# Performance work log

Measured on AMD Instinct MI355X. Metric: run time of the kernel, lower is better.

The kernel has to match this reference:

```python
import jax, jax.numpy as jnp
import numpy as np


def setup_inputs() -> dict:
    key = jax.random.key(0)
    k1, k2, k3, k4, k5 = jax.random.split(key, 5)
    B, S, H, F, E = 2, 512, 1024, 3584, 8
    scale_in = 1.0 / np.sqrt(H)
    scale_ff = 1.0 / np.sqrt(F)
    return {
        "hidden_states": jax.random.normal(k1, (B, S, H), dtype=jnp.float32),
        "gate_w": jax.random.normal(k2, (E, H), dtype=jnp.float32) * scale_in,
        "w1": jax.random.normal(k3, (E, F, H), dtype=jnp.float32) * scale_in,
        "w2": jax.random.normal(k4, (E, H, F), dtype=jnp.float32) * scale_ff,
        "w3": jax.random.normal(k5, (E, F, H), dtype=jnp.float32) * scale_in,
    }


TOP_K = 2


def reference(hidden_states, gate_w, w1, w2, w3):
    B, S, H = hidden_states.shape
    E = gate_w.shape[0]
    x = hidden_states.reshape(B * S, H)  # [T, H]
    T = x.shape[0]

    # Router: softmax in fp32, top-2 selection, renormalize selected weights.
    router_logits = x @ gate_w.T  # [T, E]
    probs = jax.nn.softmax(router_logits.astype(jnp.float32), axis=-1)
    top_vals, top_idx = jax.lax.top_k(probs, TOP_K)  # [T, K]
    top_vals = top_vals / jnp.sum(top_vals, axis=-1, keepdims=True)
    top_vals = top_vals.astype(x.dtype)

    # Dense routing-weight matrix [T, E]: weight if selected else 0
    # (equivalent to the one-hot expert_mask + index_add combine).
    dense_w = jnp.zeros((T, E), dtype=x.dtype).at[
        jnp.arange(T)[:, None], top_idx
    ].add(top_vals)

    # Expert SwiGLU MLPs, batched over the expert axis.
    h1 = jnp.einsum("th,efh->etf", x, w1)  # [E, T, F]
    h3 = jnp.einsum("th,efh->etf", x, w3)  # [E, T, F]
    y = jnp.einsum("etf,ehf->eth", jax.nn.silu(h1) * h3, w2)  # [E, T, H]

    # Weighted combine across experts.
    out = jnp.einsum("eth,te->th", y, dense_w)  # [T, H]
    return out.reshape(B, S, H), router_logits
```

## Files before the change

### kernel.cpp

```cpp
#include <hip/hip_runtime.h>
#include <hip/hip_bf16.h>

typedef __bf16 v8bf __attribute__((ext_vector_type(8)));
typedef __bf16 v4bf __attribute__((ext_vector_type(4)));
typedef float  f32x4 __attribute__((ext_vector_type(4)));
typedef unsigned int u32;

#define NTOK 1024
#define HDIM 1024
#define FDIM 3584
#define NEXP 8
#define NPAIR 2048
#define MAXT 16
#define KSPLIT2 4
#define KPER2 (FDIM / KSPLIT2)

#define OFF_COUNTS   0
#define OFF_OFFSETS  64
#define OFF_NT1      128
#define OFF_T1E      192
#define OFF_T1M      320
#define OFF_TOKIDX   2048
#define OFF_TOKWT    (2048 + 4*NPAIR)
#define OFF_PAIRTOK  (OFF_TOKWT + 4*NPAIR)
#define OFF_PAIRWT   (OFF_PAIRTOK + 4*NPAIR)
#define OFF_SLOTOF   (OFF_PAIRWT + 4*NPAIR)
#define OFF_XB       65536
#define OFF_ACT      (OFF_XB + 2ull*NTOK*HDIM)
#define OFF_Y        (OFF_ACT + 2ull*NPAIR*FDIM)
#define YSTRIDE      ((size_t)NPAIR * HDIM)

static __device__ inline v4bf cvt4(float4 f) {
    v4bf r;
    r[0] = (__bf16)f.x; r[1] = (__bf16)f.y; r[2] = (__bf16)f.z; r[3] = (__bf16)f.w;
    return r;
}

static __device__ inline v8bf pack8(f32x4 lo, f32x4 hi) {
    v8bf r;
    r[0] = (__bf16)lo[0]; r[1] = (__bf16)lo[1]; r[2] = (__bf16)lo[2]; r[3] = (__bf16)lo[3];
    r[4] = (__bf16)hi[0]; r[5] = (__bf16)hi[1]; r[6] = (__bf16)hi[2]; r[7] = (__bf16)hi[3];
    return r;
}

#define FENCE() asm volatile("" ::: "memory")
#define BARRIER() do { FENCE(); __builtin_amdgcn_s_barrier(); FENCE(); } while (0)
#define WAITVM0() asm volatile("s_waitcnt vmcnt(0)" ::: "memory")
#define WAITLGKM0() asm volatile("s_waitcnt lgkmcnt(0)" ::: "memory")

#define DMA16(SRC, DST) \
    __builtin_amdgcn_global_load_lds((const __attribute__((address_space(1))) u32*)(SRC), \
                                     (__attribute__((address_space(3))) u32*)(DST), 16, 0, 0)

__global__ __launch_bounds__(256) void moe_cvtx(const float* __restrict__ x,
                                                __bf16* __restrict__ xb)
{
    const size_t i = ((size_t)blockIdx.x * 256 + threadIdx.x) * 4;
    float4 v = *(const float4*)(x + i);
    *(v4bf*)(xb + i) = cvt4(v);
}

__global__ __launch_bounds__(256) void moe_router(
    const float* __restrict__ x, const float* __restrict__ gw,
    float* __restrict__ logits, int* __restrict__ counts,
    int* __restrict__ tok_idx, float* __restrict__ tok_wt)
{
    const int lane = threadIdx.x & 63;
    const int wv = threadIdx.x >> 6;
    const int t = blockIdx.x * 4 + wv;
    const float* xr = x + (size_t)t * HDIM;

    float acc[NEXP];
#pragma unroll
    for (int e = 0; e < NEXP; ++e) acc[e] = 0.f;
#pragma unroll
    for (int j = 0; j < 4; ++j) {
        int h = lane * 4 + j * 256;
        float4 xv = *(const float4*)(xr + h);
#pragma unroll
        for (int e = 0; e < NEXP; ++e) {
            float4 g = *(const float4*)(gw + e * HDIM + h);
            acc[e] += xv.x * g.x + xv.y * g.y + xv.z * g.z + xv.w * g.w;
        }
    }
#pragma unroll
    for (int e = 0; e < NEXP; ++e) {
#pragma unroll
        for (int s = 32; s > 0; s >>= 1) acc[e] += __shfl_xor(acc[e], s);
    }
    if (lane == 0) {
#pragma unroll
        for (int e = 0; e < NEXP; ++e) logits[t * NEXP + e] = acc[e];
        int i0 = 0;
#pragma unroll
        for (int e = 1; e < NEXP; ++e) if (acc[e] > acc[i0]) i0 = e;
        int i1 = (i0 == 0) ? 1 : 0;
#pragma unroll
        for (int e = 0; e < NEXP; ++e) if (e != i0 && acc[e] > acc[i1]) i1 = e;
        float w0 = 1.f / (1.f + expf(acc[i1] - acc[i0]));
        float w1 = 1.f - w0;
        tok_idx[2 * t] = i0; tok_idx[2 * t + 1] = i1;
        tok_wt[2 * t] = w0;  tok_wt[2 * t + 1] = w1;
        atomicAdd(&counts[i0], 1);
        atomicAdd(&counts[i1], 1);
    }
}

__global__ void moe_scatter(const int* __restrict__ counts, const int* __restrict__ tok_idx,
                            const float* __restrict__ tok_wt, int* __restrict__ offsets,
                            int* __restrict__ pair_token, float* __restrict__ pair_wt,
                            int* __restrict__ slot_of,
                            int* __restrict__ t1e, int* __restrict__ t1m, int* __restrict__ nt1)
{
    __shared__ int cur[NEXP];
    const int tid = threadIdx.x;
    if (tid == 0) {
        int run = 0, n1 = 0;
        for (int e = 0; e < NEXP; ++e) {
            offsets[e] = run; cur[e] = run;
            for (int m0 = 0; m0 < counts[e]; m0 += 256) { t1e[n1] = e; t1m[n1] = m0; ++n1; }
            run += counts[e];
        }
        *nt1 = n1;
    }
    __syncthreads();
    for (int p = tid; p < 2 * NTOK; p += blockDim.x) {
        int e = tok_idx[p];
        int s = atomicAdd(&cur[e], 1);
        pair_token[s] = p >> 1;
        pair_wt[s] = tok_wt[p];
        slot_of[p] = s;
    }
}

__global__ __launch_bounds__(256, 2) void moe_gemm1(
    const __bf16* __restrict__ xb, const float* __restrict__ w1g,
    const float* __restrict__ w3g, const int* __restrict__ counts,
    const int* __restrict__ offsets, const int* __restrict__ pair_token,
    const int* __restrict__ t1e, const int* __restrict__ t1m,
    const int* __restrict__ nt1,
    __bf16* __restrict__ act)
{
    const int ty = blockIdx.y;
    if (ty >= *nt1) return;
    const int e = t1e[ty];
    const int m0 = t1m[ty];
    const int Me = counts[e];
    const int rows = min(256, Me - m0);
    const int slot0 = offsets[e] + m0;
    const int n0 = blockIdx.x * 64;

    __shared__ __align__(16) __bf16 As[256 * 32];
    __shared__ __align__(16) float  B1s[64 * 32];
    __shared__ __align__(16) float  B3s[64 * 32];

    const int tid = threadIdx.x;
    const int lane = tid & 63;
    const int wv = tid >> 6;
    const int ln4 = lane >> 4;
    const int lr = lane & 15;
    const int wm = (wv >> 1) * 128;
    const int wn = (wv & 1) * 32;

    f32x4 acc1[8][2], acc3[8][2];
#pragma unroll
    for (int i = 0; i < 8; ++i)
#pragma unroll
        for (int j = 0; j < 2; ++j) {
            acc1[i][j] = (f32x4){0.f, 0.f, 0.f, 0.f};
            acc3[i][j] = (f32x4){0.f, 0.f, 0.f, 0.f};
        }

    const char* asrc[4];
#pragma unroll
    for (int i = 0; i < 4; ++i) {
        int c = i * 256 + tid;
        int r = c >> 2;
        int rr = (r < rows) ? r : 0;
        int sj = (c & 3) ^ ((r ^ (r >> 2)) & 3);
        asrc[i] = (const char*)(xb + (size_t)pair_token[slot0 + rr] * HDIM) + sj * 16;
    }
    const char* bsrc[2];
#pragma unroll
    for (int i = 0; i < 2; ++i) {
        int c = i * 256 + tid;
        int r = c >> 3;
        int sj = (c & 7) ^ (r & 7);
        bsrc[i] = (const char*)(w1g + ((size_t)e * FDIM + n0 + r) * HDIM) + sj * 16;
    }
    const ptrdiff_t d31b = (const char*)w3g - (const char*)w1g;

#define DMA_ALL1(K0) do { \
    _Pragma("unroll") \
    for (int i = 0; i < 4; ++i) \
        DMA16(asrc[i] + (size_t)(K0) * 64, (char*)As + (i * 256 + wv * 64) * 16); \
    _Pragma("unroll") \
    for (int i = 0; i < 2; ++i) { \
        DMA16(bsrc[i] + (size_t)(K0) * 128,        (char*)B1s + (i * 256 + wv * 64) * 16); \
        DMA16(bsrc[i] + d31b + (size_t)(K0) * 128, (char*)B3s + (i * 256 + wv * 64) * 16); \
    } } while (0)

    int aoff[8];
#pragma unroll
    for (int i = 0; i < 8; ++i) {
        int row = wm + i * 16 + lr;
        aoff[i] = row * 64 + ((ln4 ^ ((row ^ (row >> 2)) & 3)) * 16);
    }
    int blo[2], bhi[2];
#pragma unroll
    for (int i = 0; i < 2; ++i) {
        int row = wn + i * 16 + lr;
        blo[i] = row * 128 + (((ln4 * 2) ^ (row & 7)) * 16);
        bhi[i] = row * 128 + (((ln4 * 2 + 1) ^ (row & 7)) * 16);
    }

#define CMP1() do { \
    v8bf af[8], b1f[2], b3f[2]; \
    _Pragma("unroll") \
    for (int i = 0; i < 2; ++i) { \
        b1f[i] = pack8(*(const f32x4*)((const char*)B1s + blo[i]), \
                       *(const f32x4*)((const char*)B1s + bhi[i])); \
        b3f[i] = pack8(*(const f32x4*)((const char*)B3s + blo[i]), \
                       *(const f32x4*)((const char*)B3s + bhi[i])); } \
    _Pragma("unroll") \
    for (int i = 0; i < 8; ++i) af[i] = *(const v8bf*)((const char*)As + aoff[i]); \
    _Pragma("unroll") \
    for (int mi = 0; mi < 8; ++mi) { _Pragma("unroll") \
        for (int ni = 0; ni < 2; ++ni) { \
            acc1[mi][ni] = __builtin_amdgcn_mfma_f32_16x16x32_bf16(af[mi], b1f[ni], acc1[mi][ni], 0, 0, 0); \
            acc3[mi][ni] = __builtin_amdgcn_mfma_f32_16x16x32_bf16(af[mi], b3f[ni], acc3[mi][ni], 0, 0, 0); } } \
    } while (0)

    DMA_ALL1(0);
    for (int ks = 0; ks < HDIM / 32; ++ks) {
        WAITVM0();
        BARRIER();
        CMP1();
        WAITLGKM0();
        BARRIER();
        if (ks + 1 < HDIM / 32) DMA_ALL1(ks + 1);
    }
#undef DMA_ALL1
#undef CMP1

    const int rj = ln4 * 4;
#pragma unroll
    for (int mi = 0; mi < 8; ++mi) {
#pragma unroll
        for (int j = 0; j < 4; ++j) {
            int rm = wm + mi * 16 + rj + j;
            if (rm < rows) {
                size_t rowoff = (size_t)(slot0 + rm) * FDIM + n0 + wn;
#pragma unroll
                for (int ni = 0; ni < 2; ++ni) {
                    float h1 = acc1[mi][ni][j];
                    float h3 = acc3[mi][ni][j];
                    float sv = (h1 / (1.f + __expf(-h1))) * h3;
                    act[rowoff + ni * 16 + lr] = (__bf16)sv;
                }
            }
        }
    }
}

__global__ __launch_bounds__(256, 2) void moe_gemm2(
    const __bf16* __restrict__ act, const float* __restrict__ w2g,
    const int* __restrict__ counts, const int* __restrict__ offsets,
    const int* __restrict__ t1e, const int* __restrict__ t1m,
    const int* __restrict__ nt1,
    float* __restrict__ y)
{
    const int ty = blockIdx.y;
    if (ty >= *nt1) return;
    const int e = t1e[ty];
    const int m0 = t1m[ty];
    const int Me = counts[e];
    const int rows = min(256, Me - m0);
    const int slot0 = offsets[e] + m0;
    const int n0 = blockIdx.x * 64;
    const int kz = blockIdx.z;
    float* yout = y + (size_t)kz * YSTRIDE;
    const size_t kbase = (size_t)kz * KPER2;

    __shared__ __align__(16) __bf16 As[256 * 32];
    __shared__ __align__(16) float  Bs[64 * 32];

    const int tid = threadIdx.x;
    const int lane = tid & 63;
    const int wv = tid >> 6;
    const int ln4 = lane >> 4;
    const int lr = lane & 15;
    const int wm = (wv >> 1) * 128;
    const int wn = (wv & 1) * 32;

    f32x4 acc[8][2];
#pragma unroll
    for (int i = 0; i < 8; ++i)
#pragma unroll
        for (int j = 0; j < 2; ++j) acc[i][j] = (f32x4){0.f, 0.f, 0.f, 0.f};

    const char* asrc[4];
#pragma unroll
    for (int i = 0; i < 4; ++i) {
        int c = i * 256 + tid;
        int r = c >> 2;
        int rr = (r < rows) ? r : 0;
        int sj = (c & 3) ^ ((r ^ (r >> 2)) & 3);
        asrc[i] = (const char*)(act + (size_t)(slot0 + rr) * FDIM + kbase) + sj * 16;
    }
    const char* bsrc[2];
#pragma unroll
    for (int i = 0; i < 2; ++i) {
        int c = i * 256 + tid;
        int r = c >> 3;
        int sj = (c & 7) ^ (r & 7);
        bsrc[i] = (const char*)(w2g + ((size_t)e * HDIM + n0 + r) * FDIM + kbase) + sj * 16;
    }

#define DMA_ALL2(K0) do { \
    _Pragma("unroll") \
    for (int i = 0; i < 4; ++i) \
        DMA16(asrc[i] + (size_t)(K0) * 64, (char*)As + (i * 256 + wv * 64) * 16); \
    _Pragma("unroll") \
    for (int i = 0; i < 2; ++i) \
        DMA16(bsrc[i] + (size_t)(K0) * 128, (char*)Bs + (i * 256 + wv * 64) * 16); \
    } while (0)

    int aoff[8];
#pragma unroll
    for (int i = 0; i < 8; ++i) {
        int row = wm + i * 16 + lr;
        aoff[i] = row * 64 + ((ln4 ^ ((row ^ (row >> 2)) & 3)) * 16);
    }
    int blo[2], bhi[2];
#pragma unroll
    for (int i = 0; i < 2; ++i) {
        int row = wn + i * 16 + lr;
        blo[i] = row * 128 + (((ln4 * 2) ^ (row & 7)) * 16);
        bhi[i] = row * 128 + (((ln4 * 2 + 1) ^ (row & 7)) * 16);
    }

#define CMP2() do { \
    v8bf af[8], bf[2]; \
    _Pragma("unroll") \
    for (int i = 0; i < 2; ++i) \
        bf[i] = pack8(*(const f32x4*)((const char*)Bs + blo[i]), \
                      *(const f32x4*)((const char*)Bs + bhi[i])); \
    _Pragma("unroll") \
    for (int i = 0; i < 8; ++i) af[i] = *(const v8bf*)((const char*)As + aoff[i]); \
    _Pragma("unroll") \
    for (int mi = 0; mi < 8; ++mi) { _Pragma("unroll") \
        for (int ni = 0; ni < 2; ++ni) \
            acc[mi][ni] = __builtin_amdgcn_mfma_f32_16x16x32_bf16(af[mi], bf[ni], acc[mi][ni], 0, 0, 0); } \
    } while (0)

    DMA_ALL2(0);
    for (int ks = 0; ks < KPER2 / 32; ++ks) {
        WAITVM0();
        BARRIER();
        CMP2();
        WAITLGKM0();
        BARRIER();
        if (ks + 1 < KPER2 / 32) DMA_ALL2(ks + 1);
    }
#undef DMA_ALL2
#undef CMP2

    const int rj = ln4 * 4;
#pragma unroll
    for (int mi = 0; mi < 8; ++mi) {
#pragma unroll
        for (int j = 0; j < 4; ++j) {
            int rm = wm + mi * 16 + rj + j;
            if (rm < rows) {
                size_t rowoff = (size_t)(slot0 + rm) * HDIM + n0 + wn;
#pragma unroll
                for (int ni = 0; ni < 2; ++ni)
                    yout[rowoff + ni * 16 + lr] = acc[mi][ni][j];
            }
        }
    }
}

__global__ __launch_bounds__(256) void moe_combine(
    const float* __restrict__ y, const int* __restrict__ slot_of,
    const float* __restrict__ pair_wt, float* __restrict__ out)
{
    const int t = blockIdx.x;
    const int tid = threadIdx.x;
    const int s0 = slot_of[2 * t];
    const int s1 = slot_of[2 * t + 1];
    const float w0 = pair_wt[s0];
    const float w1 = pair_wt[s1];
    float4 a = {0.f, 0.f, 0.f, 0.f}, b = {0.f, 0.f, 0.f, 0.f};
#pragma unroll
    for (int k = 0; k < KSPLIT2; ++k) {
        const float4 ak = *(const float4*)(y + k * YSTRIDE + (size_t)s0 * HDIM + tid * 4);
        const float4 bk = *(const float4*)(y + k * YSTRIDE + (size_t)s1 * HDIM + tid * 4);
        a.x += ak.x; a.y += ak.y; a.z += ak.z; a.w += ak.w;
        b.x += bk.x; b.y += bk.y; b.z += bk.z; b.w += bk.w;
    }
    float4 o;
    o.x = w0 * a.x + w1 * b.x;
    o.y = w0 * a.y + w1 * b.y;
    o.z = w0 * a.z + w1 * b.z;
    o.w = w0 * a.w + w1 * b.w;
    *(float4*)(out + (size_t)t * HDIM + tid * 4) = o;
}

extern "C" void kernel_launch(void* const* d_in, const int* in_sizes, int n_in,
                              void* d_out, int out_size, void* d_ws, size_t ws_size,
                              hipStream_t stream) {
    const float* x   = (const float*)d_in[0];
    const float* gw  = (const float*)d_in[1];
    const float* w1  = (const float*)d_in[2];
    const float* w2  = (const float*)d_in[3];
    const float* w3  = (const float*)d_in[4];

    float* out    = (float*)d_out;
    float* logits = out + (size_t)NTOK * HDIM;

    char* ws = (char*)d_ws;
    int*    counts     = (int*)(ws + OFF_COUNTS);
    int*    offsets    = (int*)(ws + OFF_OFFSETS);
    int*    nt1        = (int*)(ws + OFF_NT1);
    int*    t1e        = (int*)(ws + OFF_T1E);
    int*    t1m        = (int*)(ws + OFF_T1M);
    int*    tok_idx    = (int*)(ws + OFF_TOKIDX);
    float*  tok_wt     = (float*)(ws + OFF_TOKWT);
    int*    pair_token = (int*)(ws + OFF_PAIRTOK);
    float*  pair_wt    = (float*)(ws + OFF_PAIRWT);
    int*    slot_of    = (int*)(ws + OFF_SLOTOF);
    __bf16* xb         = (__bf16*)(ws + OFF_XB);
    __bf16* act        = (__bf16*)(ws + OFF_ACT);
    float*  yb         = (float*)(ws + OFF_Y);

    hipMemsetAsync(counts, 0, 64, stream);

    moe_cvtx<<<dim3(NTOK * HDIM / 1024), dim3(256), 0, stream>>>(x, xb);
    moe_router<<<dim3(NTOK / 4), dim3(256), 0, stream>>>(x, gw, logits, counts, tok_idx, tok_wt);
    moe_scatter<<<dim3(1), dim3(256), 0, stream>>>(counts, tok_idx, tok_wt, offsets,
                                                   pair_token, pair_wt, slot_of,
                                                   t1e, t1m, nt1);
    moe_gemm1<<<dim3(FDIM / 64, MAXT), dim3(256), 0, stream>>>(
        xb, w1, w3, counts, offsets, pair_token, t1e, t1m, nt1, act);
    moe_gemm2<<<dim3(HDIM / 64, MAXT, KSPLIT2), dim3(256), 0, stream>>>(
        act, w2, counts, offsets, t1e, t1m, nt1, yb);
    moe_combine<<<dim3(NTOK), dim3(256), 0, stream>>>(yb, slot_of, pair_wt, out);
}
```

Before: 238.3 us.

## Double K-step depth per stage and narrow GEMM1 N-tile in MoE GEMMs

Both expert GEMMs now stage 64-wide K slices per barrier pair instead of 32, which halves the number of loop iterations and synchronisations. The shared-memory swizzles are reworked for the wider rows. GEMM1 also shrinks its N tile from 64 to 32 columns and launches twice as many blocks, which cuts accumulator registers and gives more parallelism. The trade-offs are larger LDS use per block, which may lower occupancy, and more redundant A-tile loads in GEMM1.

```diff
diff --git a/kernel.cpp b/kernel.cpp
--- a/kernel.cpp
+++ b/kernel.cpp
@@ -148,11 +148,11 @@
     const int Me = counts[e];
     const int rows = min(256, Me - m0);
     const int slot0 = offsets[e] + m0;
-    const int n0 = blockIdx.x * 64;
-
-    __shared__ __align__(16) __bf16 As[256 * 32];
-    __shared__ __align__(16) float  B1s[64 * 32];
-    __shared__ __align__(16) float  B3s[64 * 32];
+    const int n0 = blockIdx.x * 32;
+
+    __shared__ __align__(16) __bf16 As[256 * 64];
+    __shared__ __align__(16) float  B1s[32 * 64];
+    __shared__ __align__(16) float  B3s[32 * 64];
 
     const int tid = threadIdx.x;
     const int lane = tid & 63;
@@ -160,85 +160,81 @@
     const int ln4 = lane >> 4;
     const int lr = lane & 15;
     const int wm = (wv >> 1) * 128;
-    const int wn = (wv & 1) * 32;
-
-    f32x4 acc1[8][2], acc3[8][2];
-#pragma unroll
-    for (int i = 0; i < 8; ++i)
-#pragma unroll
-        for (int j = 0; j < 2; ++j) {
-            acc1[i][j] = (f32x4){0.f, 0.f, 0.f, 0.f};
-            acc3[i][j] = (f32x4){0.f, 0.f, 0.f, 0.f};
-        }
-
-    const char* asrc[4];
-#pragma unroll
-    for (int i = 0; i < 4; ++i) {
+    const int wn = (wv & 1) * 16;
+
+    f32x4 acc1[8], acc3[8];
+#pragma unroll
+    for (int i = 0; i < 8; ++i) {
+        acc1[i] = (f32x4){0.f, 0.f, 0.f, 0.f};
+        acc3[i] = (f32x4){0.f, 0.f, 0.f, 0.f};
+    }
+
+    const char* asrc[8];
+#pragma unroll
+    for (int i = 0; i < 8; ++i) {
         int c = i * 256 + tid;
-        int r = c >> 2;
+        int r = c >> 3;
         int rr = (r < rows) ? r : 0;
-        int sj = (c & 3) ^ ((r ^ (r >> 2)) & 3);
+        int sj = (c & 7) ^ (r & 7);
         asrc[i] = (const char*)(xb + (size_t)pair_token[slot0 + rr] * HDIM) + sj * 16;
     }
     const char* bsrc[2];
 #pragma unroll
     for (int i = 0; i < 2; ++i) {
         int c = i * 256 + tid;
-        int r = c >> 3;
-        int sj = (c & 7) ^ (r & 7);
+        int r = c >> 4;
+        int sj = (c & 15) ^ (r & 15);
         bsrc[i] = (const char*)(w1g + ((size_t)e * FDIM + n0 + r) * HDIM) + sj * 16;
     }
     const ptrdiff_t d31b = (const char*)w3g - (const char*)w1g;
 
 #define DMA_ALL1(K0) do { \
     _Pragma("unroll") \
-    for (int i = 0; i < 4; ++i) \
-        DMA16(asrc[i] + (size_t)(K0) * 64, (char*)As + (i * 256 + wv * 64) * 16); \
+    for (int i = 0; i < 8; ++i) \
+        DMA16(asrc[i] + (size_t)(K0) * 128, (char*)As + (i * 256 + wv * 64) * 16); \
     _Pragma("unroll") \
     for (int i = 0; i < 2; ++i) { \
-        DMA16(bsrc[i] + (size_t)(K0) * 128,        (char*)B1s + (i * 256 + wv * 64) * 16); \
-        DMA16(bsrc[i] + d31b + (size_t)(K0) * 128, (char*)B3s + (i * 256 + wv * 64) * 16); \
+        DMA16(bsrc[i] + (size_t)(K0) * 256,        (char*)B1s + (i * 256 + wv * 64) * 16); \
+        DMA16(bsrc[i] + d31b + (size_t)(K0) * 256, (char*)B3s + (i * 256 + wv * 64) * 16); \
     } } while (0)
 
-    int aoff[8];
+    int abase[8], axor[8];
 #pragma unroll
     for (int i = 0; i < 8; ++i) {
         int row = wm + i * 16 + lr;
-        aoff[i] = row * 64 + ((ln4 ^ ((row ^ (row >> 2)) & 3)) * 16);
-    }
-    int blo[2], bhi[2];
-#pragma unroll
-    for (int i = 0; i < 2; ++i) {
-        int row = wn + i * 16 + lr;
-        blo[i] = row * 128 + (((ln4 * 2) ^ (row & 7)) * 16);
-        bhi[i] = row * 128 + (((ln4 * 2 + 1) ^ (row & 7)) * 16);
+        abase[i] = row * 128;
+        axor[i] = (row & 7) << 4;
+    }
+    int bbase, bxor;
+    {
+        int row = wn + lr;
+        bbase = row * 256;
+        bxor = (row & 15) << 4;
     }
 
 #define CMP1() do { \
-    v8bf af[8], b1f[2], b3f[2]; \
-    _Pragma("unroll") \
-    for (int i = 0; i < 2; ++i) { \
-        b1f[i] = pack8(*(const f32x4*)((const char*)B1s + blo[i]), \
-                       *(const f32x4*)((const char*)B1s + bhi[i])); \
-        b3f[i] = pack8(*(const f32x4*)((const char*)B3s + blo[i]), \
-                       *(const f32x4*)((const char*)B3s + bhi[i])); } \
-    _Pragma("unroll") \
-    for (int i = 0; i < 8; ++i) af[i] = *(const v8bf*)((const char*)As + aoff[i]); \
-    _Pragma("unroll") \
-    for (int mi = 0; mi < 8; ++mi) { _Pragma("unroll") \
-        for (int ni = 0; ni < 2; ++ni) { \
-            acc1[mi][ni] = __builtin_amdgcn_mfma_f32_16x16x32_bf16(af[mi], b1f[ni], acc1[mi][ni], 0, 0, 0); \
-            acc3[mi][ni] = __builtin_amdgcn_mfma_f32_16x16x32_bf16(af[mi], b3f[ni], acc3[mi][ni], 0, 0, 0); } } \
-    } while (0)
+    _Pragma("unroll") \
+    for (int ksub = 0; ksub < 2; ++ksub) { \
+        int in0 = ksub * 128 + ln4 * 32; \
+        v8bf b1f = pack8(*(const f32x4*)((const char*)B1s + bbase + ((in0) ^ bxor)), \
+                         *(const f32x4*)((const char*)B1s + bbase + ((in0 + 16) ^ bxor))); \
+        v8bf b3f = pack8(*(const f32x4*)((const char*)B3s + bbase + ((in0) ^ bxor)), \
+                         *(const f32x4*)((const char*)B3s + bbase + ((in0 + 16) ^ bxor))); \
+        _Pragma("unroll") \
+        for (int mi = 0; mi < 8; ++mi) { \
+            v8bf af = *(const v8bf*)((const char*)As + abase[mi] + ((ksub * 64 + ln4 * 16) ^ axor[mi])); \
+            acc1[mi] = __builtin_amdgcn_mfma_f32_16x16x32_bf16(af, b1f, acc1[mi], 0, 0, 0); \
+            acc3[mi] = __builtin_amdgcn_mfma_f32_16x16x32_bf16(af, b3f, acc3[mi], 0, 0, 0); \
+        } } } while (0)
 
     DMA_ALL1(0);
-    for (int ks = 0; ks < HDIM / 32; ++ks) {
+    for (int ks = 0; ks < HDIM / 64; ++ks) {
         WAITVM0();
         BARRIER();
         CMP1();
         WAITLGKM0();
         BARRIER();
-        if (ks + 1 < HDIM / 32) DMA_ALL1(ks + 1);
+        if (ks + 1 < HDIM / 64) DMA_ALL1(ks + 1);
     }
 #undef DMA_ALL1
 #undef CMP1
@@ -251,13 +247,10 @@
             int rm = wm + mi * 16 + rj + j;
             if (rm < rows) {
                 size_t rowoff = (size_t)(slot0 + rm) * FDIM + n0 + wn;
-#pragma unroll
-                for (int ni = 0; ni < 2; ++ni) {
-                    float h1 = acc1[mi][ni][j];
-                    float h3 = acc3[mi][ni][j];
-                    float sv = (h1 / (1.f + __expf(-h1))) * h3;
-                    act[rowoff + ni * 16 + lr] = (__bf16)sv;
-                }
+                float h1 = acc1[mi][j];
+                float h3 = acc3[mi][j];
+                float sv = (h1 / (1.f + __expf(-h1))) * h3;
+                act[rowoff + lr] = (__bf16)sv;
             }
         }
     }
@@ -282,8 +275,8 @@
     float* yout = y + (size_t)kz * YSTRIDE;
     const size_t kbase = (size_t)kz * KPER2;
 
-    __shared__ __align__(16) __bf16 As[256 * 32];
-    __shared__ __align__(16) float  Bs[64 * 32];
+    __shared__ __align__(16) __bf16 As[256 * 64];
+    __shared__ __align__(16) float  Bs[64 * 64];
 
     const int tid = threadIdx.x;
     const int lane = tid & 63;
@@ -299,69 +292,73 @@
 #pragma unroll
         for (int j = 0; j < 2; ++j) acc[i][j] = (f32x4){0.f, 0.f, 0.f, 0.f};
 
-    const char* asrc[4];
+    const char* asrc[8];
+#pragma unroll
+    for (int i = 0; i < 8; ++i) {
+        int c = i * 256 + tid;
+        int r = c >> 3;
+        int rr = (r < rows) ? r : 0;
+        int sj = (c & 7) ^ (r & 7);
+        asrc[i] = (const char*)(act + (size_t)(slot0 + rr) * FDIM + kbase) + sj * 16;
+    }
+    const char* bsrc[4];
 #pragma unroll
     for (int i = 0; i < 4; ++i) {
         int c = i * 256 + tid;
-        int r = c >> 2;
-        int rr = (r < rows) ? r : 0;
-        int sj = (c & 3) ^ ((r ^ (r >> 2)) & 3);
-        asrc[i] = (const char*)(act + (size_t)(slot0 + rr) * FDIM + kbase) + sj * 16;
-    }
-    const char* bsrc[2];
-#pragma unroll
-    for (int i = 0; i < 2; ++i) {
-        int c = i * 256 + tid;
-        int r = c >> 3;
-        int sj = (c & 7) ^ (r & 7);
+        int r = c >> 4;
+        int sj = (c & 15) ^ (r & 15);
         bsrc[i] = (const char*)(w2g + ((size_t)e * HDIM + n0 + r) * FDIM + kbase) + sj * 16;
     }
 
 #define DMA_ALL2(K0) do { \
     _Pragma("unroll") \
+    for (int i = 0; i < 8; ++i) \
+        DMA16(asrc[i] + (size_t)(K0) * 128, (char*)As + (i * 256 + wv * 64) * 16); \
+    _Pragma("unroll") \
     for (int i = 0; i < 4; ++i) \
-        DMA16(asrc[i] + (size_t)(K0) * 64, (char*)As + (i * 256 + wv * 64) * 16); \
-    _Pragma("unroll") \
-    for (int i = 0; i < 2; ++i) \
-        DMA16(bsrc[i] + (size_t)(K0) * 128, (char*)Bs + (i * 256 + wv * 64) * 16); \
+        DMA16(bsrc[i] + (size_t)(K0) * 256, (char*)Bs + (i * 256 + wv * 64) * 16); \
     } while (0)
 
-    int aoff[8];
+    int abase[8], axor[8];
 #pragma unroll
     for (int i = 0; i < 8; ++i) {
         int row = wm + i * 16 + lr;
-        aoff[i] = row * 64 + ((ln4 ^ ((row ^ (row >> 2)) & 3)) * 16);
-    }
-    int blo[2], bhi[2];
+        abase[i] = row * 128;
+        axor[i] = (row & 7) << 4;
+    }
+    int bbase[2], bxor[2];
 #pragma unroll
     for (int i = 0; i < 2; ++i) {
         int row = wn + i * 16 + lr;
-        blo[i] = row * 128 + (((ln4 * 2) ^ (row & 7)) * 16);
-        bhi[i] = row * 128 + (((ln4 * 2 + 1) ^ (row & 7)) * 16);
+        bbase[i] = row * 256;
+        bxor[i] = (row & 15) << 4;
     }
 
 #define CMP2() do { \
-    v8bf af[8], bf[2]; \
-    _Pragma("unroll") \
-    for (int i = 0; i < 2; ++i) \
-        bf[i] = pack8(*(const f32x4*)((const char*)Bs + blo[i]), \
-                      *(const f32x4*)((const char*)Bs + bhi[i])); \
-    _Pragma("unroll") \
-    for (int i = 0; i < 8; ++i) af[i] = *(const v8bf*)((const char*)As + aoff[i]); \
-    _Pragma("unroll") \
-    for (int mi = 0; mi < 8; ++mi) { _Pragma("unroll") \
-        for (int ni = 0; ni < 2; ++ni) \
-            acc[mi][ni] = __builtin_amdgcn_mfma_f32_16x16x32_bf16(af[mi], bf[ni], acc[mi][ni], 0, 0, 0); } \
-    } while (0)
+    _Pragma("unroll") \
+    for (int ksub = 0; ksub < 2; ++ksub) { \
+        v8bf bf[2]; \
+        _Pragma("unroll") \
+        for (int ni = 0; ni < 2; ++ni) { \
+            int in0 = ksub * 128 + ln4 * 32; \
+            bf[ni] = pack8(*(const f32x4*)((const char*)Bs + bbase[ni] + ((in0) ^ bxor[ni])), \
+                           *(const f32x4*)((const char*)Bs + bbase[ni] + ((in0 + 16) ^ bxor[ni]))); } \
+        _Pragma("unroll") \
+        for (int mi = 0; mi < 8; ++mi) { \
+            v8bf af = *(const v8bf*)((const char*)As + abase[mi] + ((ksub * 64 + ln4 * 16) ^ axor[mi])); \
+            _Pragma("unroll") \
+            for (int ni = 0; ni < 2; ++ni) \
+                acc[mi][ni] = __builtin_amdgcn_mfma_f32_16x16x32_bf16(af, bf[ni], acc[mi][ni], 0, 0, 0); \
+        } } } while (0)
 
     DMA_ALL2(0);
-    for (int ks = 0; ks < KPER2 / 32; ++ks) {
+    for (int ks = 0; ks < KPER2 / 64; ++ks) {
         WAITVM0();
         BARRIER();
         CMP2();
         WAITLGKM0();
         BARRIER();
-        if (ks + 1 < KPER2 / 32) DMA_ALL2(ks + 1);
+        if (ks + 1 < KPER2 / 64) DMA_ALL2(ks + 1);
     }
 #undef DMA_ALL2
 #undef CMP2
@@ -442,7 +439,7 @@
     moe_scatter<<<dim3(1), dim3(256), 0, stream>>>(counts, tok_idx, tok_wt, offsets,
                                                    pair_token, pair_wt, slot_of,
                                                    t1e, t1m, nt1);
-    moe_gemm1<<<dim3(FDIM / 64, MAXT), dim3(256), 0, stream>>>(
+    moe_gemm1<<<dim3(FDIM / 32, MAXT), dim3(256), 0, stream>>>(
         xb, w1, w3, counts, offsets, pair_token, t1e, t1m, nt1, act);
     moe_gemm2<<<dim3(HDIM / 64, MAXT, KSPLIT2), dim3(256), 0, stream>>>(
         act, w2, counts, offsets, t1e, t1m, nt1, yb);
```

Result: faster. 192.1 us (-19.4%).

## Double-buffer expert GEMMs with register-staged bf16 weight tiles and larger blocks

Applied to the files above, without the earlier changes.

Both expert GEMM kernels move to 512-thread blocks with 128-wide N tiles and a 64-deep K step. The A tile is double-buffered in LDS through async global-to-LDS DMA. Weight tiles are now loaded into registers two steps ahead and converted to bf16 once before the LDS store, instead of being stored as fp32 and packed by every wave. The aim is to overlap global loads with MFMA work, cut barriers per K, and remove redundant fp32-to-bf16 conversion. The costs are higher register pressure, since weight prefetch sets sit alongside 64 accumulators, and a larger LDS footprint that may limit occupancy; s_setprio is also added around the compute.

```diff
diff --git a/kernel.cpp b/kernel.cpp
--- a/kernel.cpp
+++ b/kernel.cpp
@@ -14,6 +14,8 @@
 #define MAXT 16
 #define KSPLIT2 4
 #define KPER2 (FDIM / KSPLIT2)
+#define NS1 (HDIM / 64)
+#define NS2 (KPER2 / 64)
 
 #define OFF_COUNTS   0
 #define OFF_OFFSETS  64
@@ -45,7 +47,7 @@
 
 #define FENCE() asm volatile("" ::: "memory")
 #define BARRIER() do { FENCE(); __builtin_amdgcn_s_barrier(); FENCE(); } while (0)
-#define WAITVM0() asm volatile("s_waitcnt vmcnt(0)" ::: "memory")
+#define WAITVM(N) asm volatile("s_waitcnt vmcnt(" #N ")" ::: "memory")
 #define WAITLGKM0() asm volatile("s_waitcnt lgkmcnt(0)" ::: "memory")
 
 #define DMA16(SRC, DST) \
@@ -133,7 +135,7 @@
     }
 }
 
-__global__ __launch_bounds__(256, 2) void moe_gemm1(
+__global__ __launch_bounds__(512, 2) void moe_gemm1(
     const __bf16* __restrict__ xb, const float* __restrict__ w1g,
     const float* __restrict__ w3g, const int* __restrict__ counts,
     const int* __restrict__ offsets, const int* __restrict__ pair_token,
@@ -148,19 +150,19 @@
     const int Me = counts[e];
     const int rows = min(256, Me - m0);
     const int slot0 = offsets[e] + m0;
-    const int n0 = blockIdx.x * 64;
-
-    __shared__ __align__(16) __bf16 As[256 * 32];
-    __shared__ __align__(16) float  B1s[64 * 32];
-    __shared__ __align__(16) float  B3s[64 * 32];
+    const int n0 = blockIdx.x * 128;
+
+    __shared__ __align__(16) __bf16 As[2][256 * 64];
+    __shared__ __align__(16) __bf16 B1s[2][128 * 64];
+    __shared__ __align__(16) __bf16 B3s[2][128 * 64];
 
     const int tid = threadIdx.x;
     const int lane = tid & 63;
     const int wv = tid >> 6;
     const int ln4 = lane >> 4;
     const int lr = lane & 15;
-    const int wm = (wv >> 1) * 128;
-    const int wn = (wv & 1) * 32;
+    const int wm = (wv >> 2) * 128;
+    const int wn = (wv & 3) * 32;
 
     f32x4 acc1[8][2], acc3[8][2];
 #pragma unroll
@@ -174,73 +176,97 @@
     const char* asrc[4];
 #pragma unroll
     for (int i = 0; i < 4; ++i) {
-        int c = i * 256 + tid;
-        int r = c >> 2;
+        int c = i * 512 + tid;
+        int r = c >> 3;
         int rr = (r < rows) ? r : 0;
-        int sj = (c & 3) ^ ((r ^ (r >> 2)) & 3);
+        int sj = (c & 7) ^ (r & 7);
         asrc[i] = (const char*)(xb + (size_t)pair_token[slot0 + rr] * HDIM) + sj * 16;
     }
-    const char* bsrc[2];
+    const float* bsr[2];
+    int bwad[2];
 #pragma unroll
     for (int i = 0; i < 2; ++i) {
-        int c = i * 256 + tid;
+        int c = i * 512 + tid;
         int r = c >> 3;
-        int sj = (c & 7) ^ (r & 7);
-        bsrc[i] = (const char*)(w1g + ((size_t)e * FDIM + n0 + r) * HDIM) + sj * 16;
-    }
-    const ptrdiff_t d31b = (const char*)w3g - (const char*)w1g;
-
-#define DMA_ALL1(K0) do { \
+        int j = c & 7;
+        bsr[i]  = w1g + ((size_t)e * FDIM + n0 + r) * HDIM + j * 8;
+        bwad[i] = r * 128 + ((j ^ (r & 7)) * 16);
+    }
+    const ptrdiff_t d31 = w3g - w1g;
+
+    f32x4 b1A[4], b3A[4], b1B[4], b3B[4];
+
+#define DMA_A1(BUF, KS) do { _Pragma("unroll") \
+    for (int i = 0; i < 4; ++i) \
+        DMA16(asrc[i] + (size_t)(KS) * 128, (char*)&As[BUF][0] + (i * 512 + wv * 64) * 16); \
+    } while (0)
+
+#define BLD1(SET1, SET3, KS) do { _Pragma("unroll") \
+    for (int i = 0; i < 2; ++i) { \
+        SET1[i*2+0] = *(const f32x4*)(bsr[i] + (size_t)(KS) * 64); \
+        SET1[i*2+1] = *(const f32x4*)(bsr[i] + (size_t)(KS) * 64 + 4); \
+        SET3[i*2+0] = *(const f32x4*)(bsr[i] + d31 + (size_t)(KS) * 64); \
+        SET3[i*2+1] = *(const f32x4*)(bsr[i] + d31 + (size_t)(KS) * 64 + 4); \
+    } } while (0)
+
+#define STB1(SET1, SET3, BUF) do { _Pragma("unroll") \
+    for (int i = 0; i < 2; ++i) { \
+        *(v8bf*)((char*)&B1s[BUF][0] + bwad[i]) = pack8(SET1[i*2+0], SET1[i*2+1]); \
+        *(v8bf*)((char*)&B3s[BUF][0] + bwad[i]) = pack8(SET3[i*2+0], SET3[i*2+1]); \
+    } } while (0)
+
+#define CMP1(BUF) do { \
+    __builtin_amdgcn_s_setprio(1); \
     _Pragma("unroll") \
-    for (int i = 0; i < 4; ++i) \
-        DMA16(asrc[i] + (size_t)(K0) * 64, (char*)As + (i * 256 + wv * 64) * 16); \
-    _Pragma("unroll") \
-    for (int i = 0; i < 2; ++i) { \
-        DMA16(bsrc[i] + (size_t)(K0) * 128,        (char*)B1s + (i * 256 + wv * 64) * 16); \
-        DMA16(bsrc[i] + d31b + (size_t)(K0) * 128, (char*)B3s + (i * 256 + wv * 64) * 16); \
-    } } while (0)
-
-    int aoff[8];
-#pragma unroll
-    for (int i = 0; i < 8; ++i) {
-        int row = wm + i * 16 + lr;
-        aoff[i] = row * 64 + ((ln4 ^ ((row ^ (row >> 2)) & 3)) * 16);
-    }
-    int blo[2], bhi[2];
-#pragma unroll
-    for (int i = 0; i < 2; ++i) {
-        int row = wn + i * 16 + lr;
-        blo[i] = row * 128 + (((ln4 * 2) ^ (row & 7)) * 16);
-        bhi[i] = row * 128 + (((ln4 * 2 + 1) ^ (row & 7)) * 16);
-    }
-
-#define CMP1() do { \
-    v8bf af[8], b1f[2], b3f[2]; \
-    _Pragma("unroll") \
-    for (int i = 0; i < 2; ++i) { \
-        b1f[i] = pack8(*(const f32x4*)((const char*)B1s + blo[i]), \
-                       *(const f32x4*)((const char*)B1s + bhi[i])); \
-        b3f[i] = pack8(*(const f32x4*)((const char*)B3s + blo[i]), \
-                       *(const f32x4*)((const char*)B3s + bhi[i])); } \
-    _Pragma("unroll") \
-    for (int i = 0; i < 8; ++i) af[i] = *(const v8bf*)((const char*)As + aoff[i]); \
-    _Pragma("unroll") \
-    for (int mi = 0; mi < 8; ++mi) { _Pragma("unroll") \
+    for (int ksub = 0; ksub < 2; ++ksub) { \
+        v8bf b1f[2], b3f[2], af[8]; \
+        _Pragma("unroll") \
         for (int ni = 0; ni < 2; ++ni) { \
-            acc1[mi][ni] = __builtin_amdgcn_mfma_f32_16x16x32_bf16(af[mi], b1f[ni], acc1[mi][ni], 0, 0, 0); \
-            acc3[mi][ni] = __builtin_amdgcn_mfma_f32_16x16x32_bf16(af[mi], b3f[ni], acc3[mi][ni], 0, 0, 0); } } \
-    } while (0)
-
-    DMA_ALL1(0);
-    for (int ks = 0; ks < HDIM / 32; ++ks) {
-        WAITVM0();
-        BARRIER();
-        CMP1();
-        WAITLGKM0();
-        BARRIER();
-        if (ks + 1 < HDIM / 32) DMA_ALL1(ks + 1);
-    }
-#undef DMA_ALL1
+            int row = wn + ni * 16 + lr; \
+            int off = row * 128 + ((ksub * 64 + ln4 * 16) ^ ((row & 7) << 4)); \
+            b1f[ni] = *(const v8bf*)((const char*)&B1s[BUF][0] + off); \
+            b3f[ni] = *(const v8bf*)((const char*)&B3s[BUF][0] + off); } \
+        _Pragma("unroll") \
+        for (int mi = 0; mi < 8; ++mi) { \
+            int row = wm + mi * 16 + lr; \
+            af[mi] = *(const v8bf*)((const char*)&As[BUF][0] + row * 128 + \
+                                    ((ksub * 64 + ln4 * 16) ^ ((row & 7) << 4))); } \
+        _Pragma("unroll") \
+        for (int mi = 0; mi < 8; ++mi) { _Pragma("unroll") \
+            for (int ni = 0; ni < 2; ++ni) { \
+                acc1[mi][ni] = __builtin_amdgcn_mfma_f32_16x16x32_bf16(af[mi], b1f[ni], acc1[mi][ni], 0, 0, 0); \
+                acc3[mi][ni] = __builtin_amdgcn_mfma_f32_16x16x32_bf16(af[mi], b3f[ni], acc3[mi][ni], 0, 0, 0); } } \
+    } \
+    __builtin_amdgcn_s_setprio(0); \
+    } while (0)
+
+    BLD1(b1A, b3A, 0);
+    DMA_A1(0, 0);
+    BLD1(b1B, b3B, 1);
+    DMA_A1(1, 1);
+    STB1(b1A, b3A, 0);
+    WAITVM(12);
+    WAITLGKM0();
+    BARRIER();
+
+#define ITER1(KS, PBUF, SC1, SC3, SN1, SN3) do { \
+    if ((KS) == NS1 - 1) WAITVM(0); else WAITVM(12); \
+    CMP1(PBUF); \
+    if ((KS) + 2 < NS1) BLD1(SC1, SC3, (KS) + 2); \
+    if ((KS) + 1 < NS1) STB1(SN1, SN3, (PBUF) ^ 1); \
+    WAITLGKM0(); \
+    BARRIER(); \
+    if ((KS) + 2 < NS1) DMA_A1(PBUF, (KS) + 2); \
+    } while (0)
+
+    for (int ks = 0; ks < NS1; ks += 2) {
+        ITER1(ks,     0, b1A, b3A, b1B, b3B);
+        ITER1(ks + 1, 1, b1B, b3B, b1A, b3A);
+    }
+#undef ITER1
+#undef DMA_A1
+#undef BLD1
+#undef STB1
 #undef CMP1
 
     const int rj = ln4 * 4;
@@ -263,7 +289,7 @@
     }
 }
 
-__global__ __launch_bounds__(256, 2) void moe_gemm2(
+__global__ __launch_bounds__(512, 2) void moe_gemm2(
     const __bf16* __restrict__ act, const float* __restrict__ w2g,
     const int* __restrict__ counts, const int* __restrict__ offsets,
     const int* __restrict__ t1e, const int* __restrict__ t1m,
@@ -277,21 +303,21 @@
     const int Me = counts[e];
     const int rows = min(256, Me - m0);
     const int slot0 = offsets[e] + m0;
-    const int n0 = blockIdx.x * 64;
+    const int n0 = blockIdx.x * 128;
     const int kz = blockIdx.z;
     float* yout = y + (size_t)kz * YSTRIDE;
     const size_t kbase = (size_t)kz * KPER2;
 
-    __shared__ __align__(16) __bf16 As[256 * 32];
-    __shared__ __align__(16) float  Bs[64 * 32];
+    __shared__ __align__(16) __bf16 As[2][256 * 64];
+    __shared__ __align__(16) __bf16 Bs[2][128 * 64];
 
     const int tid = threadIdx.x;
     const int lane = tid & 63;
     const int wv = tid >> 6;
     const int ln4 = lane >> 4;
     const int lr = lane & 15;
-    const int wm = (wv >> 1) * 128;
-    const int wn = (wv & 1) * 32;
+    const int wm = (wv >> 2) * 128;
+    const int wn = (wv & 3) * 32;
 
     f32x4 acc[8][2];
 #pragma unroll
@@ -302,68 +328,91 @@
     const char* asrc[4];
 #pragma unroll
     for (int i = 0; i < 4; ++i) {
-        int c = i * 256 + tid;
-        int r = c >> 2;
+        int c = i * 512 + tid;
+        int r = c >> 3;
         int rr = (r < rows) ? r : 0;
-        int sj = (c & 3) ^ ((r ^ (r >> 2)) & 3);
+        int sj = (c & 7) ^ (r & 7);
         asrc[i] = (const char*)(act + (size_t)(slot0 + rr) * FDIM + kbase) + sj * 16;
     }
-    const char* bsrc[2];
+    const float* bsr[2];
+    int bwad[2];
 #pragma unroll
     for (int i = 0; i < 2; ++i) {
-        int c = i * 256 + tid;
+        int c = i * 512 + tid;
         int r = c >> 3;
-        int sj = (c & 7) ^ (r & 7);
-        bsrc[i] = (const char*)(w2g + ((size_t)e * HDIM + n0 + r) * FDIM + kbase) + sj * 16;
-    }
-
-#define DMA_ALL2(K0) do { \
+        int j = c & 7;
+        bsr[i]  = w2g + ((size_t)e * HDIM + n0 + r) * FDIM + kbase + j * 8;
+        bwad[i] = r * 128 + ((j ^ (r & 7)) * 16);
+    }
+
+    f32x4 bA[4], bB[4];
+
+#define DMA_A2(BUF, KS) do { _Pragma("unroll") \
+    for (int i = 0; i < 4; ++i) \
+        DMA16(asrc[i] + (size_t)(KS) * 128, (char*)&As[BUF][0] + (i * 512 + wv * 64) * 16); \
+    } while (0)
+
+#define BLD2(SET, KS) do { _Pragma("unroll") \
+    for (int i = 0; i < 2; ++i) { \
+        SET[i*2+0] = *(const f32x4*)(bsr[i] + (size_t)(KS) * 64); \
+        SET[i*2+1] = *(const f32x4*)(bsr[i] + (size_t)(KS) * 64 + 4); \
+    } } while (0)
+
+#define STB2(SET, BUF) do { _Pragma("unroll") \
+    for (int i = 0; i < 2; ++i) \
+        *(v8bf*)((char*)&Bs[BUF][0] + bwad[i]) = pack8(SET[i*2+0], SET[i*2+1]); \
+    } while (0)
+
+#define CMP2(BUF) do { \
+    __builtin_amdgcn_s_setprio(1); \
     _Pragma("unroll") \
-    for (int i = 0; i < 4; ++i) \
-        DMA16(asrc[i] + (size_t)(K0) * 64, (char*)As + (i * 256 + wv * 64) * 16); \
-    _Pragma("unroll") \
-    for (int i = 0; i < 2; ++i) \
-        DMA16(bsrc[i] + (size_t)(K0) * 128, (char*)Bs + (i * 256 + wv * 64) * 16); \
-    } while (0)
-
-    int aoff[8];
-#pragma unroll
-    for (int i = 0; i < 8; ++i) {
-        int row = wm + i * 16 + lr;
-        aoff[i] = row * 64 + ((ln4 ^ ((row ^ (row >> 2)) & 3)) * 16);
-    }
-    int blo[2], bhi[2];
-#pragma unroll
-    for (int i = 0; i < 2; ++i) {
-        int row = wn + i * 16 + lr;
-        blo[i] = row * 128 + (((ln4 * 2) ^ (row & 7)) * 16);
-        bhi[i] = row * 128 + (((ln4 * 2 + 1) ^ (row & 7)) * 16);
-    }
-
-#define CMP2() do { \
-    v8bf af[8], bf[2]; \
-    _Pragma("unroll") \
-    for (int i = 0; i < 2; ++i) \
-        bf[i] = pack8(*(const f32x4*)((const char*)Bs + blo[i]), \
-                      *(const f32x4*)((const char*)Bs + bhi[i])); \
-    _Pragma("unroll") \
-    for (int i = 0; i < 8; ++i) af[i] = *(const v8bf*)((const char*)As + aoff[i]); \
-    _Pragma("unroll") \
-    for (int mi = 0; mi < 8; ++mi) { _Pragma("unroll") \
-        for (int ni = 0; ni < 2; ++ni) \
-            acc[mi][ni] = __builtin_amdgcn_mfma_f32_16x16x32_bf16(af[mi], bf[ni], acc[mi][ni], 0, 0, 0); } \
-    } while (0)
-
-    DMA_ALL2(0);
-    for (int ks = 0; ks < KPER2 / 32; ++ks) {
-        WAITVM0();
-        BARRIER();
-        CMP2();
-        WAITLGKM0();
-        BARRIER();
-        if (ks + 1 < KPER2 / 32) DMA_ALL2(ks + 1);
-    }
-#undef DMA_ALL2
+    for (int ksub = 0; ksub < 2; ++ksub) { \
+        v8bf bf[2], af[8]; \
+        _Pragma("unroll") \
+        for (int ni = 0; ni < 2; ++ni) { \
+            int row = wn + ni * 16 + lr; \
+            bf[ni] = *(const v8bf*)((const char*)&Bs[BUF][0] + row * 128 + \
+                                    ((ksub * 64 + ln4 * 16) ^ ((row & 7) << 4))); } \
+        _Pragma("unroll") \
+        for (int mi = 0; mi < 8; ++mi) { \
+            int row = wm + mi * 16 + lr; \
+            af[mi] = *(const v8bf*)((const char*)&As[BUF][0] + row * 128 + \
+                                    ((ksub * 64 + ln4 * 16) ^ ((row & 7) << 4))); } \
+        _Pragma("unroll") \
+        for (int mi = 0; mi < 8; ++mi) { _Pragma("unroll") \
+            for (int ni = 0; ni < 2; ++ni) \
+                acc[mi][ni] = __builtin_amdgcn_mfma_f32_16x16x32_bf16(af[mi], bf[ni], acc[mi][ni], 0, 0, 0); } \
+    } \
+    __builtin_amdgcn_s_setprio(0); \
+    } while (0)
+
+    BLD2(bA, 0);
+    DMA_A2(0, 0);
+    BLD2(bB, 1);
+    DMA_A2(1, 1);
+    STB2(bA, 0);
+    WAITVM(8);
+    WAITLGKM0();
+    BARRIER();
+
+#define ITER2(KS, PBUF, SC, SN) do { \
+    if ((KS) == NS2 - 1) WAITVM(0); else WAITVM(8); \
+    CMP2(PBUF); \
+    if ((KS) + 2 < NS2) BLD2(SC, (KS) + 2); \
+    if ((KS) + 1 < NS2) STB2(SN, (PBUF) ^ 1); \
+    WAITLGKM0(); \
+    BARRIER(); \
+    if ((KS) + 2 < NS2) DMA_A2(PBUF, (KS) + 2); \
+    } while (0)
+
+    for (int ks = 0; ks < NS2; ks += 2) {
+        ITER2(ks,     0, bA, bB);
+        ITER2(ks + 1, 1, bB, bA);
+    }
+#undef ITER2
+#undef DMA_A2
+#undef BLD2
+#undef STB2
 #undef CMP2
 
     const int rj = ln4 * 4;
@@ -442,9 +491,9 @@
     moe_scatter<<<dim3(1), dim3(256), 0, stream>>>(counts, tok_idx, tok_wt, offsets,
                                                    pair_token, pair_wt, slot_of,
                                                    t1e, t1m, nt1);
-    moe_gemm1<<<dim3(FDIM / 64, MAXT), dim3(256), 0, stream>>>(
+    moe_gemm1<<<dim3(FDIM / 128, MAXT), dim3(512), 0, stream>>>(
         xb, w1, w3, counts, offsets, pair_token, t1e, t1m, nt1, act);
-    moe_gemm2<<<dim3(HDIM / 64, MAXT, KSPLIT2), dim3(256), 0, stream>>>(
+    moe_gemm2<<<dim3(HDIM / 128, MAXT, KSPLIT2), dim3(512), 0, stream>>>(
         act, w2, counts, offsets, t1e, t1m, nt1, yb);
     moe_combine<<<dim3(NTOK), dim3(256), 0, stream>>>(yb, slot_of, pair_wt, out);
 }
```

Result: slower. 314.8 us (+32.1%).

## Double-buffer LDS in both expert GEMMs and widen the second GEMM tile

Applied to the files above, without the earlier changes.

Both grouped GEMMs now use two LDS buffers and prefetch two k-steps ahead. Each iteration waits only for the older batch of async global-to-LDS loads (vmcnt 8), so loading the next tile overlaps the MFMA work on the current one. The MFMA section is wrapped in s_setprio, and the LDS swizzle is simplified. The second GEMM moves to 128-wide N tiles, which doubles its accumulators, and its K split goes from 4 to 7. This targets load latency and B-tile reuse, at the cost of double the LDS per block, more registers and more partial-sum traffic for the combine step.

```diff
diff --git a/kernel.cpp b/kernel.cpp
--- a/kernel.cpp
+++ b/kernel.cpp
@@ -12,8 +12,10 @@
 #define NEXP 8
 #define NPAIR 2048
 #define MAXT 16
-#define KSPLIT2 4
+#define KSPLIT2 7
 #define KPER2 (FDIM / KSPLIT2)
+#define NS1 (HDIM / 32)
+#define NS2 (KPER2 / 32)
 
 #define OFF_COUNTS   0
 #define OFF_OFFSETS  64
@@ -45,7 +47,7 @@
 
 #define FENCE() asm volatile("" ::: "memory")
 #define BARRIER() do { FENCE(); __builtin_amdgcn_s_barrier(); FENCE(); } while (0)
-#define WAITVM0() asm volatile("s_waitcnt vmcnt(0)" ::: "memory")
+#define WAITVM(N) asm volatile("s_waitcnt vmcnt(" #N ")" ::: "memory")
 #define WAITLGKM0() asm volatile("s_waitcnt lgkmcnt(0)" ::: "memory")
 
 #define DMA16(SRC, DST) \
@@ -150,9 +152,9 @@
     const int slot0 = offsets[e] + m0;
     const int n0 = blockIdx.x * 64;
 
-    __shared__ __align__(16) __bf16 As[256 * 32];
-    __shared__ __align__(16) float  B1s[64 * 32];
-    __shared__ __align__(16) float  B3s[64 * 32];
+    __shared__ __align__(16) __bf16 As[2][256 * 32];
+    __shared__ __align__(16) float  B1s[2][64 * 32];
+    __shared__ __align__(16) float  B3s[2][64 * 32];
 
     const int tid = threadIdx.x;
     const int lane = tid & 63;
@@ -177,7 +179,7 @@
         int c = i * 256 + tid;
         int r = c >> 2;
         int rr = (r < rows) ? r : 0;
-        int sj = (c & 3) ^ ((r ^ (r >> 2)) & 3);
+        int sj = (c & 3) ^ (r & 3);
         asrc[i] = (const char*)(xb + (size_t)pair_token[slot0 + rr] * HDIM) + sj * 16;
     }
     const char* bsrc[2];
@@ -190,57 +192,62 @@
     }
     const ptrdiff_t d31b = (const char*)w3g - (const char*)w1g;
 
-#define DMA_ALL1(K0) do { \
+#define DMA1(BUF, KS) do { \
     _Pragma("unroll") \
     for (int i = 0; i < 4; ++i) \
-        DMA16(asrc[i] + (size_t)(K0) * 64, (char*)As + (i * 256 + wv * 64) * 16); \
+        DMA16(asrc[i] + (size_t)(KS) * 64, (char*)&As[BUF][0] + (i * 256 + wv * 64) * 16); \
     _Pragma("unroll") \
     for (int i = 0; i < 2; ++i) { \
-        DMA16(bsrc[i] + (size_t)(K0) * 128,        (char*)B1s + (i * 256 + wv * 64) * 16); \
-        DMA16(bsrc[i] + d31b + (size_t)(K0) * 128, (char*)B3s + (i * 256 + wv * 64) * 16); \
+        DMA16(bsrc[i] + (size_t)(KS) * 128,        (char*)&B1s[BUF][0] + (i * 256 + wv * 64) * 16); \
+        DMA16(bsrc[i] + d31b + (size_t)(KS) * 128, (char*)&B3s[BUF][0] + (i * 256 + wv * 64) * 16); \
     } } while (0)
 
     int aoff[8];
 #pragma unroll
     for (int i = 0; i < 8; ++i) {
         int row = wm + i * 16 + lr;
-        aoff[i] = row * 64 + ((ln4 ^ ((row ^ (row >> 2)) & 3)) * 16);
+        aoff[i] = row * 64 + ((ln4 ^ (row & 3)) << 4);
     }
     int blo[2], bhi[2];
 #pragma unroll
     for (int i = 0; i < 2; ++i) {
         int row = wn + i * 16 + lr;
-        blo[i] = row * 128 + (((ln4 * 2) ^ (row & 7)) * 16);
-        bhi[i] = row * 128 + (((ln4 * 2 + 1) ^ (row & 7)) * 16);
-    }
-
-#define CMP1() do { \
-    v8bf af[8], b1f[2], b3f[2]; \
-    _Pragma("unroll") \
-    for (int i = 0; i < 2; ++i) { \
-        b1f[i] = pack8(*(const f32x4*)((const char*)B1s + blo[i]), \
-                       *(const f32x4*)((const char*)B1s + bhi[i])); \
-        b3f[i] = pack8(*(const f32x4*)((const char*)B3s + blo[i]), \
-                       *(const f32x4*)((const char*)B3s + bhi[i])); } \
-    _Pragma("unroll") \
-    for (int i = 0; i < 8; ++i) af[i] = *(const v8bf*)((const char*)As + aoff[i]); \
+        blo[i] = row * 128 + (((ln4 * 2) ^ (row & 7)) << 4);
+        bhi[i] = row * 128 + (((ln4 * 2 + 1) ^ (row & 7)) << 4);
+    }
+
+#define CMP1(BUF) do { \
+    const char* Ab = (const char*)&As[BUF][0]; \
+    const char* B1b = (const char*)&B1s[BUF][0]; \
+    const char* B3b = (const char*)&B3s[BUF][0]; \
+    v8bf b1f[2], b3f[2], af[8]; \
+    __builtin_amdgcn_s_setprio(1); \
+    _Pragma("unroll") \
+    for (int ni = 0; ni < 2; ++ni) { \
+        b1f[ni] = pack8(*(const f32x4*)(B1b + blo[ni]), *(const f32x4*)(B1b + bhi[ni])); \
+        b3f[ni] = pack8(*(const f32x4*)(B3b + blo[ni]), *(const f32x4*)(B3b + bhi[ni])); } \
+    _Pragma("unroll") \
+    for (int mi = 0; mi < 8; ++mi) af[mi] = *(const v8bf*)(Ab + aoff[mi]); \
     _Pragma("unroll") \
     for (int mi = 0; mi < 8; ++mi) { _Pragma("unroll") \
         for (int ni = 0; ni < 2; ++ni) { \
             acc1[mi][ni] = __builtin_amdgcn_mfma_f32_16x16x32_bf16(af[mi], b1f[ni], acc1[mi][ni], 0, 0, 0); \
             acc3[mi][ni] = __builtin_amdgcn_mfma_f32_16x16x32_bf16(af[mi], b3f[ni], acc3[mi][ni], 0, 0, 0); } } \
+    __builtin_amdgcn_s_setprio(0); \
     } while (0)
 
-    DMA_ALL1(0);
-    for (int ks = 0; ks < HDIM / 32; ++ks) {
-        WAITVM0();
+    DMA1(0, 0);
+    DMA1(1, 1);
+    for (int ks = 0; ks < NS1; ++ks) {
+        if (ks < NS1 - 1) WAITVM(8);
+        else              WAITVM(0);
         BARRIER();
-        CMP1();
+        CMP1(ks & 1);
         WAITLGKM0();
         BARRIER();
-        if (ks + 1 < HDIM / 32) DMA_ALL1(ks + 1);
-    }
-#undef DMA_ALL1
+        if (ks + 2 < NS1) DMA1(ks & 1, ks + 2);
+    }
+#undef DMA1
 #undef CMP1
 
     const int rj = ln4 * 4;
@@ -277,13 +284,13 @@
     const int Me = counts[e];
     const int rows = min(256, Me - m0);
     const int slot0 = offsets[e] + m0;
-    const int n0 = blockIdx.x * 64;
+    const int n0 = blockIdx.x * 128;
     const int kz = blockIdx.z;
     float* yout = y + (size_t)kz * YSTRIDE;
     const size_t kbase = (size_t)kz * KPER2;
 
-    __shared__ __align__(16) __bf16 As[256 * 32];
-    __shared__ __align__(16) float  Bs[64 * 32];
+    __shared__ __align__(16) __bf16 As[2][256 * 32];
+    __shared__ __align__(16) float  Bs[2][128 * 32];
 
     const int tid = threadIdx.x;
     const int lane = tid & 63;
@@ -291,13 +298,13 @@
     const int ln4 = lane >> 4;
     const int lr = lane & 15;
     const int wm = (wv >> 1) * 128;
-    const int wn = (wv & 1) * 32;
-
-    f32x4 acc[8][2];
+    const int wn = (wv & 1) * 64;
+
+    f32x4 acc[8][4];
 #pragma unroll
     for (int i = 0; i < 8; ++i)
 #pragma unroll
-        for (int j = 0; j < 2; ++j) acc[i][j] = (f32x4){0.f, 0.f, 0.f, 0.f};
+        for (int j = 0; j < 4; ++j) acc[i][j] = (f32x4){0.f, 0.f, 0.f, 0.f};
 
     const char* asrc[4];
 #pragma unroll
@@ -305,65 +312,68 @@
         int c = i * 256 + tid;
         int r = c >> 2;
         int rr = (r < rows) ? r : 0;
-        int sj = (c & 3) ^ ((r ^ (r >> 2)) & 3);
+        int sj = (c & 3) ^ (r & 3);
         asrc[i] = (const char*)(act + (size_t)(slot0 + rr) * FDIM + kbase) + sj * 16;
     }
-    const char* bsrc[2];
-#pragma unroll
-    for (int i = 0; i < 2; ++i) {
+    const char* bsrc[4];
+#pragma unroll
+    for (int i = 0; i < 4; ++i) {
         int c = i * 256 + tid;
         int r = c >> 3;
         int sj = (c & 7) ^ (r & 7);
         bsrc[i] = (const char*)(w2g + ((size_t)e * HDIM + n0 + r) * FDIM + kbase) + sj * 16;
     }
 
-#define DMA_ALL2(K0) do { \
-    _Pragma("unroll") \
-    for (int i = 0; i < 4; ++i) \
-        DMA16(asrc[i] + (size_t)(K0) * 64, (char*)As + (i * 256 + wv * 64) * 16); \
-    _Pragma("unroll") \
-    for (int i = 0; i < 2; ++i) \
-        DMA16(bsrc[i] + (size_t)(K0) * 128, (char*)Bs + (i * 256 + wv * 64) * 16); \
-    } while (0)
+#define DMA2(BUF, KS) do { \
+    _Pragma("unroll") \
+    for (int i = 0; i < 4; ++i) { \
+        DMA16(asrc[i] + (size_t)(KS) * 64,  (char*)&As[BUF][0] + (i * 256 + wv * 64) * 16); \
+        DMA16(bsrc[i] + (size_t)(KS) * 128, (char*)&Bs[BUF][0] + (i * 256 + wv * 64) * 16); \
+    } } while (0)
 
     int aoff[8];
 #pragma unroll
     for (int i = 0; i < 8; ++i) {
         int row = wm + i * 16 + lr;
-        aoff[i] = row * 64 + ((ln4 ^ ((row ^ (row >> 2)) & 3)) * 16);
-    }
-    int blo[2], bhi[2];
-#pragma unroll
-    for (int i = 0; i < 2; ++i) {
+        aoff[i] = row * 64 + ((ln4 ^ (row & 3)) << 4);
+    }
+    int blo[4], bhi[4];
+#pragma unroll
+    for (int i = 0; i < 4; ++i) {
         int row = wn + i * 16 + lr;
-        blo[i] = row * 128 + (((ln4 * 2) ^ (row & 7)) * 16);
-        bhi[i] = row * 128 + (((ln4 * 2 + 1) ^ (row & 7)) * 16);
-    }
-
-#define CMP2() do { \
-    v8bf af[8], bf[2]; \
-    _Pragma("unroll") \
-    for (int i = 0; i < 2; ++i) \
-        bf[i] = pack8(*(const f32x4*)((const char*)Bs + blo[i]), \
-                      *(const f32x4*)((const char*)Bs + bhi[i])); \
-    _Pragma("unroll") \
-    for (int i = 0; i < 8; ++i) af[i] = *(const v8bf*)((const char*)As + aoff[i]); \
+        blo[i] = row * 128 + (((ln4 * 2) ^ (row & 7)) << 4);
+        bhi[i] = row * 128 + (((ln4 * 2 + 1) ^ (row & 7)) << 4);
+    }
+
+#define CMP2(BUF) do { \
+    const char* Ab = (const char*)&As[BUF][0]; \
+    const char* Bb = (const char*)&Bs[BUF][0]; \
+    v8bf bf[4], af[8]; \
+    __builtin_amdgcn_s_setprio(1); \
+    _Pragma("unroll") \
+    for (int ni = 0; ni < 4; ++ni) \
+        bf[ni] = pack8(*(const f32x4*)(Bb + blo[ni]), *(const f32x4*)(Bb + bhi[ni])); \
+    _Pragma("unroll") \
+    for (int mi = 0; mi < 8; ++mi) af[mi] = *(const v8bf*)(Ab + aoff[mi]); \
     _Pragma("unroll") \
     for (int mi = 0; mi < 8; ++mi) { _Pragma("unroll") \
-        for (int ni = 0; ni < 2; ++ni) \
+        for (int ni = 0; ni < 4; ++ni) \
             acc[mi][ni] = __builtin_amdgcn_mfma_f32_16x16x32_bf16(af[mi], bf[ni], acc[mi][ni], 0, 0, 0); } \
+    __builtin_amdgcn_s_setprio(0); \
     } while (0)
 
-    DMA_ALL2(0);
-    for (int ks = 0; ks < KPER2 / 32; ++ks) {
-        WAITVM0();
+    DMA2(0, 0);
+    DMA2(1, 1);
+    for (int ks = 0; ks < NS2; ++ks) {
+        if (ks < NS2 - 1) WAITVM(8);
+        else              WAITVM(0);
         BARRIER();
-        CMP2();
+        CMP2(ks & 1);
         WAITLGKM0();
         BARRIER();
-        if (ks + 1 < KPER2 / 32) DMA_ALL2(ks + 1);
-    }
-#undef DMA_ALL2
+        if (ks + 2 < NS2) DMA2(ks & 1, ks + 2);
+    }
+#undef DMA2
 #undef CMP2
 
     const int rj = ln4 * 4;
@@ -375,7 +385,7 @@
             if (rm < rows) {
                 size_t rowoff = (size_t)(slot0 + rm) * HDIM + n0 + wn;
 #pragma unroll
-                for (int ni = 0; ni < 2; ++ni)
+                for (int ni = 0; ni < 4; ++ni)
                     yout[rowoff + ni * 16 + lr] = acc[mi][ni][j];
             }
         }
@@ -444,7 +454,7 @@
                                                    t1e, t1m, nt1);
     moe_gemm1<<<dim3(FDIM / 64, MAXT), dim3(256), 0, stream>>>(
         xb, w1, w3, counts, offsets, pair_token, t1e, t1m, nt1, act);
-    moe_gemm2<<<dim3(HDIM / 64, MAXT, KSPLIT2), dim3(256), 0, stream>>>(
+    moe_gemm2<<<dim3(HDIM / 128, MAXT, KSPLIT2), dim3(256), 0, stream>>>(
         act, w2, counts, offsets, t1e, t1m, nt1, yb);
     moe_combine<<<dim3(NTOK), dim3(256), 0, stream>>>(yb, slot_of, pair_wt, out);
 }
```

Result: faster. 224.1 us (-5.9%).
